# Kernel tuning notes

Measured on AMD Instinct MI355X. Metric: run time of the kernel, lower is better.

Reference implementation:

```python
import jax, jax.numpy as jnp
import numpy as np

B, H, NI, NQ = 4096, 1024, 4096, 2048


def setup_inputs() -> dict:
    key = jax.random.key(0)
    ks = jax.random.split(key, 12)
    state = jax.random.normal(ks[0], (B, H), jnp.float32)
    inputX = jax.random.normal(ks[1], (B, NI), jnp.float32)
    # one-hot next-question vector
    q_idx = jax.random.randint(ks[2], (B,), 0, NQ)
    inputY = jax.nn.one_hot(q_idx, NQ, dtype=jnp.float32)
    truth = jax.random.bernoulli(ks[3], 0.5, (B,)).astype(jnp.float32)
    # torch.nn.Linear default init: U(-1/sqrt(fan_in), 1/sqrt(fan_in)), weight (out,in)
    def lin(kw, kb, out_d, in_d):
        bound = 1.0 / np.sqrt(in_d)
        W = jax.random.uniform(kw, (out_d, in_d), jnp.float32, -bound, bound)
        b = jax.random.uniform(kb, (out_d,), jnp.float32, -bound, bound)
        return W, b
    W_t, b_t = lin(ks[4], ks[5], H, H)    # transfer: n_hidden -> n_hidden
    W_x, b_x = lin(ks[6], ks[7], H, NI)   # linear_x: n_input -> n_hidden
    W_y, b_y = lin(ks[8], ks[9], NQ, H)   # linear_y: n_hidden -> n_questions
    return {"state": state, "inputX": inputX, "inputY": inputY, "truth": truth,
            "W_t": W_t, "b_t": b_t, "W_x": W_x, "b_x": b_x, "W_y": W_y, "b_y": b_y}


def reference(state, inputX, inputY, truth, W_t, b_t, W_x, b_x, W_y, b_y):
    # two small linears + tanh -> new hidden state
    linM = state @ W_t.T + b_t                       # (B, H)
    linX = inputX @ W_x.T + b_x                      # (B, H)
    hidden = jnp.tanh(linM + linX)                   # (B, H)
    # prediction head: linear + sigmoid, mask-select via one-hot sum
    pred_output = jax.nn.sigmoid(hidden @ W_y.T + b_y)  # (B, NQ)
    pred = jnp.sum(pred_output * inputY, axis=1)        # (B,)
    # binary cross entropy, sum reduction; torch clamps log terms at -100
    log_p = jnp.maximum(jnp.log(pred), -100.0)
    log_1mp = jnp.maximum(jnp.log1p(-pred), -100.0)
    err = -jnp.sum(truth * log_p + (1.0 - truth) * log_1mp)
    return (pred, err, hidden)
```

## Files before the change

### kernel.cpp

```cpp
#include <hip/hip_runtime.h>
#include <stdint.h>
#include <math.h>

#define B_DIM 4096
#define H_DIM 1024
#define NI_DIM 4096
#define NQ_DIM 2048
#define K_DIM 5120
#define NKT 160

typedef __attribute__((ext_vector_type(8))) short short8;
typedef __attribute__((ext_vector_type(4))) float f32x4;

__device__ __forceinline__ unsigned short f2bf(float f) {
  unsigned u = __float_as_uint(f);
  u += 0x7FFFu + ((u >> 16) & 1u);
  return (unsigned short)(u >> 16);
}
__device__ __forceinline__ float bf2f(unsigned short s) {
  return __uint_as_float(((unsigned)s) << 16);
}
__device__ __forceinline__ unsigned pkbf(float a, float b) {
  unsigned r;
  asm("v_cvt_pk_bf16_f32 %0, %1, %2" : "=v"(r) : "v"(a), "v"(b));
  return r;
}

__device__ __forceinline__ void gload_lds16(const void* g, void* l) {
  __builtin_amdgcn_global_load_lds(
      (__attribute__((address_space(1))) void*)(uintptr_t)g,
      (__attribute__((address_space(3))) void*)l, 16, 0, 0);
}

__global__ __launch_bounds__(256) void cast_w(
    const float* __restrict__ Wt, const float* __restrict__ Wx,
    short* __restrict__ Wc) {
  __shared__ __align__(16) short lds[4096];
  const int bt = blockIdx.x;
  const int rowTile = bt / NKT;
  const int kt = bt % NKT;
  const float* src;
  long long srcBase;
  int cols;
  if (kt < 32) { src = Wt; cols = 1024; srcBase = (long long)kt * 32; }
  else         { src = Wx; cols = 4096; srcBase = (long long)(kt - 32) * 32; }
  const int tid = threadIdx.x;
#pragma unroll
  for (int half = 0; half < 2; ++half) {
    int c = tid + half * 256;
    int r = c >> 2, s = c & 3;
    long long sa = ((long long)(rowTile * 128 + r)) * cols + srcBase + s * 8;
    float4 v0 = *(const float4*)(src + sa);
    float4 v1 = *(const float4*)(src + sa + 4);
    short8 o;
    o[0] = (short)f2bf(v0.x); o[1] = (short)f2bf(v0.y);
    o[2] = (short)f2bf(v0.z); o[3] = (short)f2bf(v0.w);
    o[4] = (short)f2bf(v1.x); o[5] = (short)f2bf(v1.y);
    o[6] = (short)f2bf(v1.z); o[7] = (short)f2bf(v1.w);
    *(short8*)(&lds[(s * 128 + r) * 8]) = o;
  }
  __syncthreads();
  short* dtile = Wc + (((long long)rowTile * NKT + kt) * 512) * 8;
#pragma unroll
  for (int half = 0; half < 2; ++half) {
    int c = tid + half * 256;
    *(short8*)(dtile + c * 8) = *(const short8*)(&lds[c * 8]);
  }
}

__device__ __forceinline__ int ep_swz(int col, int rw) {
  int byte = col * 256 + rw * 2;
  byte ^= ((col ^ (col >> 3)) & 7) << 4;
  return byte;
}

__global__ __launch_bounds__(256, 4) void gemm_splitk(
    const float* __restrict__ state, const float* __restrict__ inputX,
    const short* __restrict__ Wc, short* __restrict__ P, int ntk) {
  __shared__ __align__(16) short SH[16384];
  const int tid = threadIdx.x;
  const int lane = tid & 63;
  const int wid = tid >> 6;
  const int wm = wid >> 1, wn = wid & 1;
  const int fr = lane & 15, fq = lane >> 4;

  const int nwg = gridDim.x;
  const int orig = blockIdx.x;
  const int cpx = nwg >> 3;
  const int swz = (orig & 7) * cpx + (orig >> 3);
  const int bz = swz >> 8;
  const int bm = (swz >> 3) & 31;
  const int bn = swz & 7;
  const int kt0 = bz * ntk;

  const int r = tid >> 1, hh = tid & 1;
  const float* qS = state  + (long long)(bm * 128 + r) * 1024 + hh * 16;
  const float* qX = inputX + (long long)(bm * 128 + r) * 4096 + hh * 16;

  const int c0 = tid, c1 = tid + 256;
  const short* gB = Wc + (((long long)bn * NKT + kt0) << 12);

  f32x4 acc[4][4] = {};
  float4 rA0, rA1, rA2, rA3;

  {
    int ktg = kt0;
    const float* q = (ktg < 32) ? (qS + ktg * 32) : (qX + (ktg - 32) * 32);
    rA0 = *(const float4*)(q);
    rA1 = *(const float4*)(q + 4);
    rA2 = *(const float4*)(q + 8);
    rA3 = *(const float4*)(q + 12);
    gload_lds16(gB + c0 * 8, &SH[8192 + c0 * 8]);
    gload_lds16(gB + c1 * 8, &SH[8192 + c1 * 8]);
    uint4 w0, w1;
    w0.x = pkbf(rA0.x, rA0.y); w0.y = pkbf(rA0.z, rA0.w);
    w0.z = pkbf(rA1.x, rA1.y); w0.w = pkbf(rA1.z, rA1.w);
    w1.x = pkbf(rA2.x, rA2.y); w1.y = pkbf(rA2.z, rA2.w);
    w1.z = pkbf(rA3.x, rA3.y); w1.w = pkbf(rA3.z, rA3.w);
    *(uint4*)(&SH[((2 * hh) * 128 + r) * 8]) = w0;
    *(uint4*)(&SH[((2 * hh + 1) * 128 + r) * 8]) = w1;
  }
  __syncthreads();

  int cur = 0;
  for (int t = 0; t < ntk; ++t) {
    if (t + 1 < ntk) {
      int ktg = kt0 + t + 1;
      const float* q = (ktg < 32) ? (qS + ktg * 32) : (qX + (ktg - 32) * 32);
      rA0 = *(const float4*)(q);
      rA1 = *(const float4*)(q + 4);
      rA2 = *(const float4*)(q + 8);
      rA3 = *(const float4*)(q + 12);
      const short* nB = gB + (long long)(t + 1) * 4096;
      short* lB = &SH[8192 + (cur ^ 1) * 4096];
      gload_lds16(nB + c0 * 8, lB + c0 * 8);
      gload_lds16(nB + c1 * 8, lB + c1 * 8);
    }
    const short* a_base = &SH[cur * 4096];
    const short* b_base = &SH[8192 + cur * 4096];
    short8 av[4], bv[4];
#pragma unroll
    for (int i = 0; i < 4; i++) {
      av[i] = *(const short8*)(a_base + (fq * 128 + wm * 64 + i * 16 + fr) * 8);
      bv[i] = *(const short8*)(b_base + (fq * 128 + wn * 64 + i * 16 + fr) * 8);
    }
#pragma unroll
    for (int mi = 0; mi < 4; mi++)
#pragma unroll
      for (int ni = 0; ni < 4; ni++)
        acc[mi][ni] = __builtin_amdgcn_mfma_f32_16x16x32_bf16(
            av[mi], bv[ni], acc[mi][ni], 0, 0, 0);
    if (t + 1 < ntk) {
      short* lA = &SH[(cur ^ 1) * 4096];
      uint4 w0, w1;
      w0.x = pkbf(rA0.x, rA0.y); w0.y = pkbf(rA0.z, rA0.w);
      w0.z = pkbf(rA1.x, rA1.y); w0.w = pkbf(rA1.z, rA1.w);
      w1.x = pkbf(rA2.x, rA2.y); w1.y = pkbf(rA2.z, rA2.w);
      w1.z = pkbf(rA3.x, rA3.y); w1.w = pkbf(rA3.z, rA3.w);
      *(uint4*)(lA + ((2 * hh) * 128 + r) * 8) = w0;
      *(uint4*)(lA + ((2 * hh + 1) * 128 + r) * 8) = w1;
    }
    __syncthreads();
    cur ^= 1;
  }

#pragma unroll
  for (int ni = 0; ni < 4; ni++) {
    int col = wn * 64 + ni * 16 + fr;
#pragma unroll
    for (int mi = 0; mi < 4; mi++) {
      int rw = wm * 64 + mi * 16 + fq * 4;
      unsigned lo = (unsigned)f2bf(acc[mi][ni][0]) |
                    ((unsigned)f2bf(acc[mi][ni][1]) << 16);
      unsigned hi = (unsigned)f2bf(acc[mi][ni][2]) |
                    ((unsigned)f2bf(acc[mi][ni][3]) << 16);
      uint2 pk; pk.x = lo; pk.y = hi;
      *(uint2*)((char*)SH + ep_swz(col, rw)) = pk;
    }
  }
  __syncthreads();
  short* Pp = P + (long long)bz * B_DIM * H_DIM;
#pragma unroll
  for (int h = 0; h < 8; ++h) {
    int chunk = tid + h * 256;
    int rr = chunk >> 4;
    int j = chunk & 15;
    short8 o;
#pragma unroll
    for (int k = 0; k < 8; ++k) {
      o[k] = *(const short*)((char*)SH + ep_swz(j * 8 + k, rr));
    }
    *(short8*)(Pp + (long long)(bm * 128 + rr) * H_DIM + bn * 128 + j * 8) = o;
  }
}

__global__ __launch_bounds__(256) void fuse_row(
    const short* __restrict__ P, const float* __restrict__ bt,
    const float* __restrict__ bx, const float* __restrict__ Y,
    const float* __restrict__ truth, const float* __restrict__ Wy,
    const float* __restrict__ by, float* __restrict__ predOut,
    float* __restrict__ hidden, float* __restrict__ bce, int S) {
  const int b = blockIdx.x;
  const int tid = threadIdx.x;
  __shared__ int s_cnt;
  __shared__ int s_idx[8];
  __shared__ float s_val[8];
  __shared__ float s_red[4];
  if (tid == 0) s_cnt = 0;

  const int c = tid * 4;
  float s0 = 0.f, s1 = 0.f, s2 = 0.f, s3 = 0.f;
  for (int z = 0; z < S; ++z) {
    const short* Pr = P + ((long long)z * B_DIM + b) * H_DIM + c;
    uint2 u = *(const uint2*)Pr;
    s0 += bf2f((unsigned short)(u.x & 0xffff));
    s1 += bf2f((unsigned short)(u.x >> 16));
    s2 += bf2f((unsigned short)(u.y & 0xffff));
    s3 += bf2f((unsigned short)(u.y >> 16));
  }
  float4 bt4 = *(const float4*)(bt + c);
  float4 bx4 = *(const float4*)(bx + c);
  float h0 = tanhf(s0 + bt4.x + bx4.x);
  float h1 = tanhf(s1 + bt4.y + bx4.y);
  float h2 = tanhf(s2 + bt4.z + bx4.z);
  float h3 = tanhf(s3 + bt4.w + bx4.w);
  float* Hr = hidden + (long long)b * H_DIM + c;
  Hr[0] = h0; Hr[1] = h1; Hr[2] = h2; Hr[3] = h3;

  __syncthreads();
  const float4* Yr = (const float4*)(Y + (long long)b * NQ_DIM);
#pragma unroll
  for (int hh = 0; hh < NQ_DIM / 4 / 256; ++hh) {
    int j = tid + hh * 256;
    float4 v = Yr[j];
    if (v.x != 0.0f) { int p = atomicAdd(&s_cnt, 1); if (p < 8) { s_idx[p] = 4 * j;     s_val[p] = v.x; } }
    if (v.y != 0.0f) { int p = atomicAdd(&s_cnt, 1); if (p < 8) { s_idx[p] = 4 * j + 1; s_val[p] = v.y; } }
    if (v.z != 0.0f) { int p = atomicAdd(&s_cnt, 1); if (p < 8) { s_idx[p] = 4 * j + 2; s_val[p] = v.z; } }
    if (v.w != 0.0f) { int p = atomicAdd(&s_cnt, 1); if (p < 8) { s_idx[p] = 4 * j + 3; s_val[p] = v.w; } }
  }
  __syncthreads();
  int cnt = s_cnt < 8 ? s_cnt : 8;
  float predv = 0.0f;
  for (int it = 0; it < cnt; ++it) {
    int q = s_idx[it];
    float4 w = *(const float4*)(Wy + (long long)q * H_DIM + c);
    float part = h0 * w.x + h1 * w.y + h2 * w.z + h3 * w.w;
#pragma unroll
    for (int off = 32; off > 0; off >>= 1) part += __shfl_down(part, off, 64);
    if ((tid & 63) == 0) s_red[tid >> 6] = part;
    __syncthreads();
    if (tid == 0) {
      float z = s_red[0] + s_red[1] + s_red[2] + s_red[3] + by[q];
      float p = 1.0f / (1.0f + expf(-z));
      predv += s_val[it] * p;
    }
    __syncthreads();
  }
  if (tid == 0) {
    predOut[b] = predv;
    float t = truth[b];
    float lp = fmaxf(logf(predv), -100.0f);
    float l1p = fmaxf(log1pf(-predv), -100.0f);
    bce[b] = -(t * lp + (1.0f - t) * l1p);
  }
}

__global__ __launch_bounds__(256) void reduce_err(
    const float* __restrict__ bce, float* __restrict__ errOut) {
  float s = 0.0f;
  for (int i = threadIdx.x; i < B_DIM; i += 256) s += bce[i];
#pragma unroll
  for (int off = 32; off > 0; off >>= 1) s += __shfl_down(s, off, 64);
  __shared__ float red[4];
  if ((threadIdx.x & 63) == 0) red[threadIdx.x >> 6] = s;
  __syncthreads();
  if (threadIdx.x == 0) errOut[0] = red[0] + red[1] + red[2] + red[3];
}

extern "C" void kernel_launch(void* const* d_in, const int* in_sizes, int n_in,
                              void* d_out, int out_size, void* d_ws, size_t ws_size,
                              hipStream_t stream) {
  (void)in_sizes; (void)n_in; (void)out_size;
  const float* state  = (const float*)d_in[0];
  const float* inputX = (const float*)d_in[1];
  const float* inputY = (const float*)d_in[2];
  const float* truth  = (const float*)d_in[3];
  const float* W_t    = (const float*)d_in[4];
  const float* b_t    = (const float*)d_in[5];
  const float* W_x    = (const float*)d_in[6];
  const float* b_x    = (const float*)d_in[7];
  const float* W_y    = (const float*)d_in[8];
  const float* b_y    = (const float*)d_in[9];

  const size_t WC_B = (size_t)H_DIM * K_DIM * 2;
  const size_t PART = (size_t)B_DIM * H_DIM * 2;

  int S = 1;
  if (ws_size >= WC_B + 4 * PART + 16384) S = 4;
  else if (ws_size >= WC_B + 2 * PART + 16384) S = 2;

  short* Wc = (short*)d_ws;
  short* P  = (short*)((char*)d_ws + WC_B);
  float* bce = (float*)((char*)d_ws + WC_B + (size_t)S * PART);

  float* predOut = (float*)d_out;
  float* errOut  = predOut + B_DIM;
  float* hidden  = predOut + B_DIM + 1;

  cast_w<<<(H_DIM / 128) * NKT, 256, 0, stream>>>(W_t, W_x, Wc);

  gemm_splitk<<<256 * S, 256, 0, stream>>>(state, inputX, Wc, P, NKT / S);

  fuse_row<<<B_DIM, 256, 0, stream>>>(P, b_t, b_x, inputY, truth, W_y, b_y,
                                      predOut, hidden, bce, S);
  reduce_err<<<1, 256, 0, stream>>>(bce, errOut);
}
```

Measured before the change: 94.76 us.

## Stage fp32 activations directly to LDS and convert to bf16 at fragment load

The GEMM kernel now copies fp32 rows of state/inputX straight into LDS with async global-to-LDS loads, using an XOR-swizzled layout, instead of loading them into registers, converting to bf16 and storing them. The bf16 conversion moves to the point where each wave reads its A fragment from LDS. This removes register staging and the synchronous convert-and-store from the main loop, so A loads can overlap compute like the B loads. In exchange, LDS use grows to 48KB, occupancy drops from 4 to 3 blocks per CU, and each A element is converted redundantly by the two waves that share it.

```diff
diff --git a/kernel.cpp b/kernel.cpp
--- a/kernel.cpp
+++ b/kernel.cpp
@@ -1,4 +1,5 @@
 #include <hip/hip_runtime.h>
+#include <hip/hip_bf16.h>
 #include <stdint.h>
 #include <math.h>
 
@@ -19,11 +20,6 @@
 }
 __device__ __forceinline__ float bf2f(unsigned short s) {
   return __uint_as_float(((unsigned)s) << 16);
-}
-__device__ __forceinline__ unsigned pkbf(float a, float b) {
-  unsigned r;
-  asm("v_cvt_pk_bf16_f32 %0, %1, %2" : "=v"(r) : "v"(a), "v"(b));
-  return r;
 }
 
 __device__ __forceinline__ void gload_lds16(const void* g, void* l) {
@@ -74,10 +70,10 @@
   return byte;
 }
 
-__global__ __launch_bounds__(256, 4) void gemm_splitk(
+__global__ __launch_bounds__(256, 3) void gemm_f32a(
     const float* __restrict__ state, const float* __restrict__ inputX,
     const short* __restrict__ Wc, short* __restrict__ P, int ntk) {
-  __shared__ __align__(16) short SH[16384];
+  __shared__ __align__(16) short SH[24576];
   const int tid = threadIdx.x;
   const int lane = tid & 63;
   const int wid = tid >> 6;
@@ -93,32 +89,33 @@
   const int bn = swz & 7;
   const int kt0 = bz * ntk;
 
-  const int r = tid >> 1, hh = tid & 1;
-  const float* qS = state  + (long long)(bm * 128 + r) * 1024 + hh * 16;
-  const float* qX = inputX + (long long)(bm * 128 + r) * 4096 + hh * 16;
-
   const int c0 = tid, c1 = tid + 256;
   const short* gB = Wc + (((long long)bn * NKT + kt0) << 12);
 
+  long long aoffS[4], aoffX[4];
+#pragma unroll
+  for (int j = 0; j < 4; ++j) {
+    int c = tid + j * 256;
+    int r = c >> 3, qp = c & 7;
+    int ql = qp ^ (r & 7);
+    long long grow = bm * 128 + r;
+    aoffS[j] = grow * 1024 + ql * 4;
+    aoffX[j] = grow * 4096 + ql * 4;
+  }
+
   f32x4 acc[4][4] = {};
-  float4 rA0, rA1, rA2, rA3;
 
   {
     int ktg = kt0;
-    const float* q = (ktg < 32) ? (qS + ktg * 32) : (qX + (ktg - 32) * 32);
-    rA0 = *(const float4*)(q);
-    rA1 = *(const float4*)(q + 4);
-    rA2 = *(const float4*)(q + 8);
-    rA3 = *(const float4*)(q + 12);
-    gload_lds16(gB + c0 * 8, &SH[8192 + c0 * 8]);
-    gload_lds16(gB + c1 * 8, &SH[8192 + c1 * 8]);
-    uint4 w0, w1;
-    w0.x = pkbf(rA0.x, rA0.y); w0.y = pkbf(rA0.z, rA0.w);
-    w0.z = pkbf(rA1.x, rA1.y); w0.w = pkbf(rA1.z, rA1.w);
-    w1.x = pkbf(rA2.x, rA2.y); w1.y = pkbf(rA2.z, rA2.w);
-    w1.z = pkbf(rA3.x, rA3.y); w1.w = pkbf(rA3.z, rA3.w);
-    *(uint4*)(&SH[((2 * hh) * 128 + r) * 8]) = w0;
-    *(uint4*)(&SH[((2 * hh + 1) * 128 + r) * 8]) = w1;
+    const float* baseS = state + (long long)ktg * 32;
+    const float* baseX = inputX + (long long)(ktg - 32) * 32;
+#pragma unroll
+    for (int j = 0; j < 4; ++j) {
+      const float* g = (ktg < 32) ? (baseS + aoffS[j]) : (baseX + aoffX[j]);
+      gload_lds16(g, &SH[(tid + j * 256) * 8]);
+    }
+    gload_lds16(gB + c0 * 8, &SH[16384 + c0 * 8]);
+    gload_lds16(gB + c1 * 8, &SH[16384 + c1 * 8]);
   }
   __syncthreads();
 
@@ -126,22 +123,34 @@
   for (int t = 0; t < ntk; ++t) {
     if (t + 1 < ntk) {
       int ktg = kt0 + t + 1;
-      const float* q = (ktg < 32) ? (qS + ktg * 32) : (qX + (ktg - 32) * 32);
-      rA0 = *(const float4*)(q);
-      rA1 = *(const float4*)(q + 4);
-      rA2 = *(const float4*)(q + 8);
-      rA3 = *(const float4*)(q + 12);
+      const float* baseS = state + (long long)ktg * 32;
+      const float* baseX = inputX + (long long)(ktg - 32) * 32;
+      short* lA = &SH[(cur ^ 1) * 8192];
+#pragma unroll
+      for (int j = 0; j < 4; ++j) {
+        const float* g = (ktg < 32) ? (baseS + aoffS[j]) : (baseX + aoffX[j]);
+        gload_lds16(g, lA + (tid + j * 256) * 8);
+      }
       const short* nB = gB + (long long)(t + 1) * 4096;
-      short* lB = &SH[8192 + (cur ^ 1) * 4096];
+      short* lB = &SH[16384 + (cur ^ 1) * 4096];
       gload_lds16(nB + c0 * 8, lB + c0 * 8);
       gload_lds16(nB + c1 * 8, lB + c1 * 8);
     }
-    const short* a_base = &SH[cur * 4096];
-    const short* b_base = &SH[8192 + cur * 4096];
+    const float4* a_base = (const float4*)&SH[cur * 8192];
+    const short* b_base = &SH[16384 + cur * 4096];
     short8 av[4], bv[4];
 #pragma unroll
     for (int i = 0; i < 4; i++) {
-      av[i] = *(const short8*)(a_base + (fq * 128 + wm * 64 + i * 16 + fr) * 8);
+      int row = wm * 64 + i * 16 + fr;
+      int e = row & 7;
+      float4 lo = a_base[row * 8 + ((2 * fq) ^ e)];
+      float4 hi = a_base[row * 8 + ((2 * fq + 1) ^ e)];
+      union { short8 s; __hip_bfloat162 h[4]; } u;
+      u.h[0] = __float22bfloat162_rn(make_float2(lo.x, lo.y));
+      u.h[1] = __float22bfloat162_rn(make_float2(lo.z, lo.w));
+      u.h[2] = __float22bfloat162_rn(make_float2(hi.x, hi.y));
+      u.h[3] = __float22bfloat162_rn(make_float2(hi.z, hi.w));
+      av[i] = u.s;
       bv[i] = *(const short8*)(b_base + (fq * 128 + wn * 64 + i * 16 + fr) * 8);
     }
 #pragma unroll
@@ -150,16 +159,6 @@
       for (int ni = 0; ni < 4; ni++)
         acc[mi][ni] = __builtin_amdgcn_mfma_f32_16x16x32_bf16(
             av[mi], bv[ni], acc[mi][ni], 0, 0, 0);
-    if (t + 1 < ntk) {
-      short* lA = &SH[(cur ^ 1) * 4096];
-      uint4 w0, w1;
-      w0.x = pkbf(rA0.x, rA0.y); w0.y = pkbf(rA0.z, rA0.w);
-      w0.z = pkbf(rA1.x, rA1.y); w0.w = pkbf(rA1.z, rA1.w);
-      w1.x = pkbf(rA2.x, rA2.y); w1.y = pkbf(rA2.z, rA2.w);
-      w1.z = pkbf(rA3.x, rA3.y); w1.w = pkbf(rA3.z, rA3.w);
-      *(uint4*)(lA + ((2 * hh) * 128 + r) * 8) = w0;
-      *(uint4*)(lA + ((2 * hh + 1) * 128 + r) * 8) = w1;
-    }
     __syncthreads();
     cur ^= 1;
   }
@@ -309,7 +308,7 @@
 
   cast_w<<<(H_DIM / 128) * NKT, 256, 0, stream>>>(W_t, W_x, Wc);
 
-  gemm_splitk<<<256 * S, 256, 0, stream>>>(state, inputX, Wc, P, NKT / S);
+  gemm_f32a<<<256 * S, 256, 0, stream>>>(state, inputX, Wc, P, NKT / S);
 
   fuse_row<<<B_DIM, 256, 0, stream>>>(P, b_t, b_x, inputY, truth, W_y, b_y,
                                       predOut, hidden, bce, S);
```

After: 111.2 us. +17.4%, slower.
